# Optimization experiments

Hardware: AMD Instinct MI355X
Metric: run time of the kernel (lower is better)

## Reference

```python
import math
import jax, jax.numpy as jnp
import numpy as np

B, H, W, DIM, HEADS, K = 4, 56, 56, 512, 16, 7


def setup_inputs() -> dict:
    key = jax.random.key(0)
    ks = jax.random.split(key, 8)
    s = 1.0 / math.sqrt(DIM)
    return {
        "hidden_states": jax.random.normal(ks[0], (B, H, W, DIM), jnp.float32),
        "Wq": jax.random.normal(ks[1], (DIM, DIM), jnp.float32) * s,
        "bq": jnp.zeros((DIM,), jnp.float32),
        "Wk": jax.random.normal(ks[2], (DIM, DIM), jnp.float32) * s,
        "bk": jnp.zeros((DIM,), jnp.float32),
        "Wv": jax.random.normal(ks[3], (DIM, DIM), jnp.float32) * s,
        "bv": jnp.zeros((DIM,), jnp.float32),
        "rpb": jax.random.normal(ks[4], (HEADS, 2 * K - 1, 2 * K - 1), jnp.float32) * 0.02,
    }


def reference(hidden_states, Wq, bq, Wk, bk, Wv, bv, rpb):
    b, h_sz, w_sz, dim = hidden_states.shape
    heads = rpb.shape[0]
    k = (rpb.shape[1] + 1) // 2  # rpb is [heads, 2k-1, 2k-1]
    d = dim // heads

    def split_heads(x):
        # [B,H,W,dim] -> [B,heads,H,W,d]  (matches transpose_for_scores permute(0,3,1,2,4))
        return x.reshape(b, h_sz, w_sz, heads, d).transpose(0, 3, 1, 2, 4)

    q = split_heads(hidden_states @ Wq.T + bq) / jnp.sqrt(jnp.asarray(d, hidden_states.dtype))
    key = split_heads(hidden_states @ Wk.T + bk)
    val = split_heads(hidden_states @ Wv.T + bv)

    half = k // 2
    ii = jnp.arange(h_sz)
    ni = jnp.clip(ii - half, 0, h_sz - k)  # neighborhood row start per query row (NATTEN edge clamping)
    jj = jnp.arange(w_sz)
    nj = jnp.clip(jj - half, 0, w_sz - k)

    # natten2dqkrpb: windowed QK with relative position bias (loop over k*k kernel offsets,
    # which mirrors the fused kernel's inner loop and avoids a [B,h,H,W,k,k,d] gather blowup)
    scores = []
    for ki in range(k):
        ridx = ni + ki                      # [H] key row index per query row
        bi = ridx - ii + (k - 1)            # [H] relative bias row index
        key_r = key[:, :, ridx]             # [B,h,H,W,d]
        rpb_r = rpb[:, bi]                  # [h,H,2k-1]
        for kj in range(k):
            cidx = nj + kj                  # [W]
            bj = cidx - jj + (k - 1)        # [W]
            key_rc = key_r[:, :, :, cidx]   # [B,h,H,W,d]
            s = jnp.einsum('bhijd,bhijd->bhij', q, key_rc)
            scores.append(s + rpb_r[:, :, bj][None])  # add bias [1,h,H,W]
    scores = jnp.stack(scores, axis=-1)     # [B,h,H,W,k*k]

    probs = jax.nn.softmax(scores, axis=-1)  # dropout p=0.0 -> identity

    # natten2dav: windowed AV
    ctx = jnp.zeros_like(q)                 # [B,h,H,W,d]
    idx = 0
    for ki in range(k):
        v_r = val[:, :, ni + ki]
        for kj in range(k):
            ctx = ctx + probs[..., idx, None] * v_r[:, :, :, nj + kj]
            idx += 1

    # permute(0,2,3,1,4) then merge heads
    return ctx.transpose(0, 2, 3, 1, 4).reshape(b, h_sz, w_sz, dim)
```

## Files before the change

### kernel.cpp

```cpp
#include <hip/hip_runtime.h>
#include <stdint.h>

typedef unsigned short u16;
typedef __bf16 bf16x8 __attribute__((ext_vector_type(8)));
typedef float f32x4 __attribute__((ext_vector_type(4)));

#define M_PIX 12544
#define DIMC  512
#define NQKV  1536

static __device__ __forceinline__ u16 f2bf(float f) {
  union { float f; uint32_t u; } x; x.f = f;
  uint32_t r = x.u + 0x7FFFu + ((x.u >> 16) & 1u);
  return (u16)(r >> 16);
}

__global__ void cast_all(const float* __restrict__ x, const float* __restrict__ Wq,
                         const float* __restrict__ Wk, const float* __restrict__ Wv,
                         u16* __restrict__ Xb, u16* __restrict__ Wc) {
  int idx = (blockIdx.x * 256 + threadIdx.x) * 4;
  const int NX = M_PIX * DIMC;
  const float* src;
  u16* dst;
  if (idx < NX) {
    src = x + idx; dst = Xb + idx;
  } else {
    int wi = idx - NX;
    if (wi >= NQKV * DIMC) return;
    int r = wi >> 9;
    int c = wi & 511;
    src = (r < 512)  ? (Wq + (size_t)r * 512 + c)
        : (r < 1024) ? (Wk + (size_t)(r - 512) * 512 + c)
                     : (Wv + (size_t)(r - 1024) * 512 + c);
    dst = Wc + wi;
  }
  float4 f = *(const float4*)src;
  uint32_t p0 = (uint32_t)f2bf(f.x) | ((uint32_t)f2bf(f.y) << 16);
  uint32_t p1 = (uint32_t)f2bf(f.z) | ((uint32_t)f2bf(f.w) << 16);
  *(uint2*)dst = make_uint2(p0, p1);
}

__global__ __launch_bounds__(256, 4) void gemm_qkv(
    const u16* __restrict__ A, const u16* __restrict__ Bm,
    const float* __restrict__ bq, const float* __restrict__ bk,
    const float* __restrict__ bv, u16* __restrict__ qkv) {
  __shared__ u16 sA[2][128 * 32];
  __shared__ u16 sB[2][128 * 32];
  const int t = threadIdx.x;
  const int lane = t & 63;
  const int w = t >> 6;
  const int bid = blockIdx.x;
  const int g = (bid & 7) * 147 + (bid >> 3);
  const int tile_m = (g / 12) * 128;
  const int tile_n = (g % 12) * 128;
  const int wm = (w & 1) * 64;
  const int wn = (w >> 1) * 64;
  const int quad = lane >> 4;
  const int l16 = lane & 15;

  f32x4 acc[4][4];
#pragma unroll
  for (int a = 0; a < 4; ++a)
#pragma unroll
    for (int bb = 0; bb < 4; ++bb) acc[a][bb] = (f32x4){0.f, 0.f, 0.f, 0.f};

  const int c0 = t, c1 = t + 256;
  const int r0 = c0 >> 2, ko0 = (((c0 & 3) ^ ((c0 >> 3) & 3))) * 8;
  const int r1 = c1 >> 2, ko1 = (((c1 & 3) ^ ((c1 >> 3) & 3))) * 8;
  const u16* gA0 = A + (size_t)(tile_m + r0) * DIMC + ko0;
  const u16* gA1 = A + (size_t)(tile_m + r1) * DIMC + ko1;
  const u16* gB0 = Bm + (size_t)(tile_n + r0) * DIMC + ko0;
  const u16* gB1 = Bm + (size_t)(tile_n + r1) * DIMC + ko1;
  const int ldsoff = (t & ~63) * 8;

  for (int k0 = 0; k0 < DIMC; k0 += 64) {
#pragma unroll
    for (int h = 0; h < 2; ++h) {
      __builtin_amdgcn_global_load_lds(
          (const __attribute__((address_space(1))) void*)(gA0 + k0 + h * 32),
          (__attribute__((address_space(3))) void*)(sA[h] + 0 * 2048 + ldsoff), 16, 0, 0);
      __builtin_amdgcn_global_load_lds(
          (const __attribute__((address_space(1))) void*)(gA1 + k0 + h * 32),
          (__attribute__((address_space(3))) void*)(sA[h] + 1 * 2048 + ldsoff), 16, 0, 0);
      __builtin_amdgcn_global_load_lds(
          (const __attribute__((address_space(1))) void*)(gB0 + k0 + h * 32),
          (__attribute__((address_space(3))) void*)(sB[h] + 0 * 2048 + ldsoff), 16, 0, 0);
      __builtin_amdgcn_global_load_lds(
          (const __attribute__((address_space(1))) void*)(gB1 + k0 + h * 32),
          (__attribute__((address_space(3))) void*)(sB[h] + 1 * 2048 + ldsoff), 16, 0, 0);
    }
    __syncthreads();

    const int sw8 = (quad ^ ((l16 >> 1) & 3)) * 8;
#pragma unroll
    for (int h = 0; h < 2; ++h) {
      bf16x8 af[4], bfr[4];
#pragma unroll
      for (int mt = 0; mt < 4; ++mt)
        af[mt] = *(const bf16x8*)(sA[h] + (wm + mt * 16 + l16) * 32 + sw8);
#pragma unroll
      for (int nt = 0; nt < 4; ++nt)
        bfr[nt] = *(const bf16x8*)(sB[h] + (wn + nt * 16 + l16) * 32 + sw8);
#pragma unroll
      for (int mt = 0; mt < 4; ++mt)
#pragma unroll
        for (int nt = 0; nt < 4; ++nt)
          acc[mt][nt] = __builtin_amdgcn_mfma_f32_16x16x32_bf16(bfr[nt], af[mt], acc[mt][nt], 0, 0, 0);
    }
    __syncthreads();
  }

  const float qscale = 0.17677669529663687f;
#pragma unroll
  for (int mt = 0; mt < 4; ++mt) {
    const int m = tile_m + wm + mt * 16 + l16;
#pragma unroll
    for (int nt = 0; nt < 4; ++nt) {
      const int n0 = tile_n + wn + nt * 16 + quad * 4;
      const int mat = n0 >> 9;
      const int cc = n0 & 511;
      const float* bias = (mat == 0) ? bq : (mat == 1) ? bk : bv;
      const float4 bv4 = *(const float4*)(bias + cc);
      const float scl = (mat == 0) ? qscale : 1.0f;
      u16 h0 = f2bf((acc[mt][nt][0] + bv4.x) * scl);
      u16 h1 = f2bf((acc[mt][nt][1] + bv4.y) * scl);
      u16 h2 = f2bf((acc[mt][nt][2] + bv4.z) * scl);
      u16 h3 = f2bf((acc[mt][nt][3] + bv4.w) * scl);
      uint2 pk = make_uint2((uint32_t)h0 | ((uint32_t)h1 << 16),
                            (uint32_t)h2 | ((uint32_t)h3 << 16));
      *(uint2*)(qkv + (size_t)mat * M_PIX * DIMC + (size_t)m * DIMC + cc) = pk;
    }
  }
}

__global__ __launch_bounds__(512, 4) void natten_k(const u16* __restrict__ qkv,
                                                   const float* __restrict__ rpb,
                                                   float* __restrict__ out) {
  __shared__ u16 sP[8 * 2688];
  __shared__ u16 sVt[32 * 296];
  __shared__ float sRpb[256];
  __shared__ uint32_t sTbl[320];

  const int tid = threadIdx.x;
  const int lane = tid & 63;
  const int w = tid >> 6;
  const int l16 = lane & 15;
  const int quad = lane >> 4;

  const int bid = blockIdx.x;
  const int xcd = bid & 7;
  const int idx = bid >> 3;
  const int head = idx / 14;
  const int gl = idx - head * 14;
  const int g = xcd * 14 + gl;
  const int jg = g & 3;
  const int gi = g >> 2;
  const int b = gi / 7;
  const int ig = gi - b * 7;
  const int i0 = ig * 8, j0 = jg * 14;
  int c0 = j0 - 3; c0 = c0 < 0 ? 0 : (c0 > 36 ? 36 : c0);
  int nib = i0 - 3; nib = nib < 0 ? 0 : (nib > 49 ? 49 : nib);

  const int iw = i0 + w;
  int niw = iw - 3; niw = niw < 0 ? 0 : (niw > 49 ? 49 : niw);
  const int rowoff = niw - nib;
  const int par = rowoff & 1;
  const int woff2 = rowoff * 20 - par * 4;
  const int wconst = niw - iw + 6;

  const int qv = l16 < 14 ? l16 : 13;
  const int jq = j0 + qv;
  int njq = jq - 3; njq = njq < 0 ? 0 : (njq > 49 ? 49 : njq);
  const uint32_t offq = (uint32_t)(njq - c0);
  const int Cq = wconst * 13 + (c0 - jq + 6);

  const u16* Kpl = qkv + (size_t)M_PIX * DIMC;

  union { uint4 u; bf16x8 v; } qu;
  qu.u = make_uint4(0, 0, 0, 0);
  if (l16 < 14) {
    size_t qpx = (size_t)((b * 56 + iw) * 56 + j0 + l16);
    qu.u = *(const uint4*)(qkv + qpx * DIMC + head * 32 + quad * 8);
  }
  const bf16x8 qf = qu.v;

  if (tid < 296) {
    const int pair = tid >> 1, half = tid & 1;
    const int cand0 = pair * 2;
    int r = (cand0 * 205) >> 12;
    int c = cand0 - r * 20;
    int rimg = nib + r;
    const bool ok = (rimg < 56);
    size_t px = (size_t)((b * 56 + rimg) * 56 + c0 + c);
    const u16* vsrc = Kpl + (size_t)M_PIX * DIMC + px * DIMC + head * 32 + half * 16;
    u16* vt = sVt + cand0;
#pragma unroll
    for (int dgh = 0; dgh < 2; ++dgh) {
      uint4 va = ok ? *(const uint4*)(vsrc + dgh * 8) : make_uint4(0, 0, 0, 0);
      uint4 vb = ok ? *(const uint4*)(vsrc + DIMC + dgh * 8) : make_uint4(0, 0, 0, 0);
      int d0 = (half * 2 + dgh) * 8;
      *(uint32_t*)(vt + (d0 + 0) * 296) = __builtin_amdgcn_perm(vb.x, va.x, 0x05040100u);
      *(uint32_t*)(vt + (d0 + 1) * 296) = __builtin_amdgcn_perm(vb.x, va.x, 0x07060302u);
      *(uint32_t*)(vt + (d0 + 2) * 296) = __builtin_amdgcn_perm(vb.y, va.y, 0x05040100u);
      *(uint32_t*)(vt + (d0 + 3) * 296) = __builtin_amdgcn_perm(vb.y, va.y, 0x07060302u);
      *(uint32_t*)(vt + (d0 + 4) * 296) = __builtin_amdgcn_perm(vb.z, va.z, 0x05040100u);
      *(uint32_t*)(vt + (d0 + 5) * 296) = __builtin_amdgcn_perm(vb.z, va.z, 0x07060302u);
      *(uint32_t*)(vt + (d0 + 6) * 296) = __builtin_amdgcn_perm(vb.w, va.w, 0x05040100u);
      *(uint32_t*)(vt + (d0 + 7) * 296) = __builtin_amdgcn_perm(vb.w, va.w, 0x07060302u);
    }
  }
  const float LOG2E = 1.4426950408889634f;
  if (tid < 256) sRpb[tid] = (tid < 169) ? rpb[head * 169 + tid] * LOG2E : 0.f;
  if (tid < 320) {
    int pp = tid >= 160 ? 1 : 0;
    int s = tid - pp * 160;
    int t0 = s - pp * 4;
    uint32_t e = 255u;
    if (t0 >= 0 && t0 < 140) {
      int r = (t0 * 205) >> 12;
      int c = t0 - r * 20;
      e = (uint32_t)c | ((uint32_t)(r * 13 + c) << 8);
    }
    sTbl[tid] = e;
  }

  const int pxbase = (b * 56 + nib) * 56 + c0;
  const u16* kbase = Kpl + (size_t)head * 32 + quad * 8;
  bf16x8 kreg[9];
#pragma unroll
  for (int ch = 0; ch < 9; ++ch) {
    int cand = woff2 + ch * 16 + l16;
    int r = (cand * 205) >> 12;
    int c = cand - r * 20;
    int px = pxbase + r * 56 + c;
    kreg[ch] = *(const bf16x8*)(kbase + (size_t)px * DIMC);
  }

  __syncthreads();

  u16* sPw = sP + w * 2688;
  f32x4 S[9];
  __builtin_amdgcn_s_setprio(1);
#pragma unroll
  for (int ch = 0; ch < 9; ++ch)
    S[ch] = __builtin_amdgcn_mfma_f32_16x16x32_bf16(kreg[ch], qf, (f32x4){0.f, 0.f, 0.f, 0.f}, 0, 0, 0);
  __builtin_amdgcn_s_setprio(0);

  float l = 0.f;
  const uint32_t* tb = sTbl + par * 160;
#pragma unroll
  for (int ch = 0; ch < 9; ++ch) {
    uint4 te = *(const uint4*)(tb + ch * 16 + quad * 4);
    float pv[4];
    uint32_t es[4] = {te.x, te.y, te.z, te.w};
#pragma unroll
    for (int rg = 0; rg < 4; ++rg) {
      uint32_t e = es[rg];
      uint32_t ce = e & 255u;
      bool valid = (ce - offq) < 7u;
      int ridx = (int)((e >> 8) & 255u) + Cq;
      float rbl = sRpb[ridx];
      float p = exp2f(__builtin_fmaf(S[ch][rg], LOG2E, rbl));
      p = valid ? p : 0.f;
      pv[rg] = p;
      l += p;
    }
    uint32_t plo, phi;
    asm("v_cvt_pk_bf16_f32 %0, %1, %2" : "=v"(plo) : "v"(pv[0]), "v"(pv[1]));
    asm("v_cvt_pk_bf16_f32 %0, %1, %2" : "=v"(phi) : "v"(pv[2]), "v"(pv[3]));
    *(uint2*)((char*)sPw + l16 * 336 + ch * 32 + quad * 8) = make_uint2(plo, phi);
  }
  *(uint2*)((char*)sPw + l16 * 336 + 9 * 32 + quad * 8) = make_uint2(0u, 0u);
  l += __shfl_xor(l, 16);
  l += __shfl_xor(l, 32);

  asm volatile("s_waitcnt lgkmcnt(0)" ::: "memory");
  __builtin_amdgcn_sched_barrier(0);

  f32x4 O0 = (f32x4){0.f, 0.f, 0.f, 0.f};
  f32x4 O1 = (f32x4){0.f, 0.f, 0.f, 0.f};
  __builtin_amdgcn_s_setprio(1);
#pragma unroll
  for (int c32 = 0; c32 < 5; ++c32) {
    bf16x8 pf = *(const bf16x8*)((char*)sPw + l16 * 336 + c32 * 64 + quad * 16);
    bf16x8 v0 = *(const bf16x8*)((char*)sVt + (0 + l16) * 592 + woff2 * 2 + c32 * 64 + quad * 16);
    bf16x8 v1 = *(const bf16x8*)((char*)sVt + (16 + l16) * 592 + woff2 * 2 + c32 * 64 + quad * 16);
    O0 = __builtin_amdgcn_mfma_f32_16x16x32_bf16(v0, pf, O0, 0, 0, 0);
    O1 = __builtin_amdgcn_mfma_f32_16x16x32_bf16(v1, pf, O1, 0, 0, 0);
  }
  __builtin_amdgcn_s_setprio(0);

  if (l16 < 14) {
    const float inv = __builtin_amdgcn_rcpf(l);
    float* op = out + ((size_t)((b * 56 + iw) * 56 + j0 + l16)) * DIMC + head * 32;
    *(float4*)(op + quad * 4) =
        make_float4(O0[0] * inv, O0[1] * inv, O0[2] * inv, O0[3] * inv);
    *(float4*)(op + 16 + quad * 4) =
        make_float4(O1[0] * inv, O1[1] * inv, O1[2] * inv, O1[3] * inv);
  }
}

extern "C" void kernel_launch(void* const* d_in, const int* in_sizes, int n_in,
                              void* d_out, int out_size, void* d_ws, size_t ws_size,
                              hipStream_t stream) {
  const float* x   = (const float*)d_in[0];
  const float* Wq  = (const float*)d_in[1];
  const float* bq  = (const float*)d_in[2];
  const float* Wk  = (const float*)d_in[3];
  const float* bk  = (const float*)d_in[4];
  const float* Wv  = (const float*)d_in[5];
  const float* bv  = (const float*)d_in[6];
  const float* rpb = (const float*)d_in[7];
  float* out = (float*)d_out;

  u16* Xb  = (u16*)d_ws;
  u16* Wc  = Xb + (size_t)M_PIX * DIMC;
  u16* qkv = Wc + (size_t)NQKV * DIMC;

  const int ncast = (M_PIX * DIMC + NQKV * DIMC) / 4;
  cast_all<<<(ncast + 255) / 256, 256, 0, stream>>>(x, Wq, Wk, Wv, Xb, Wc);
  gemm_qkv<<<1176, 256, 0, stream>>>(Xb, Wc, bq, bk, bv, qkv);
  natten_k<<<1792, 512, 0, stream>>>(qkv, rpb, out);
}
```

Measured before the change: 147.9 us.

## Fuse fp32-to-bf16 activation cast into QKV GEMM A-tile loads

Removes the separate cast pass over the activations. The GEMM now reads fp32 X directly, converts it with v_cvt_pk_bf16_f32 in registers, and writes swizzled bf16 into LDS; only the weights still go through a standalone cast kernel. This avoids writing and re-reading a 12.8 MB bf16 intermediate. In exchange, the A operand is no longer loaded asynchronously with global_load_lds, so the GEMM reads twice the bytes per A element (each fp32 tile is re-read by the 12 N-tiles) and spends more registers and VALU work in the load path.

```diff
diff --git a/kernel.cpp b/kernel.cpp
--- a/kernel.cpp
+++ b/kernel.cpp
@@ -15,33 +15,23 @@
   return (u16)(r >> 16);
 }
 
-__global__ void cast_all(const float* __restrict__ x, const float* __restrict__ Wq,
-                         const float* __restrict__ Wk, const float* __restrict__ Wv,
-                         u16* __restrict__ Xb, u16* __restrict__ Wc) {
-  int idx = (blockIdx.x * 256 + threadIdx.x) * 4;
-  const int NX = M_PIX * DIMC;
-  const float* src;
-  u16* dst;
-  if (idx < NX) {
-    src = x + idx; dst = Xb + idx;
-  } else {
-    int wi = idx - NX;
-    if (wi >= NQKV * DIMC) return;
-    int r = wi >> 9;
-    int c = wi & 511;
-    src = (r < 512)  ? (Wq + (size_t)r * 512 + c)
-        : (r < 1024) ? (Wk + (size_t)(r - 512) * 512 + c)
-                     : (Wv + (size_t)(r - 1024) * 512 + c);
-    dst = Wc + wi;
-  }
+__global__ void cast_w(const float* __restrict__ Wq, const float* __restrict__ Wk,
+                       const float* __restrict__ Wv, u16* __restrict__ Wc) {
+  int wi = (blockIdx.x * 256 + threadIdx.x) * 4;
+  if (wi >= NQKV * DIMC) return;
+  int r = wi >> 9;
+  int c = wi & 511;
+  const float* src = (r < 512)  ? (Wq + (size_t)r * 512 + c)
+                   : (r < 1024) ? (Wk + (size_t)(r - 512) * 512 + c)
+                                : (Wv + (size_t)(r - 1024) * 512 + c);
   float4 f = *(const float4*)src;
   uint32_t p0 = (uint32_t)f2bf(f.x) | ((uint32_t)f2bf(f.y) << 16);
   uint32_t p1 = (uint32_t)f2bf(f.z) | ((uint32_t)f2bf(f.w) << 16);
-  *(uint2*)dst = make_uint2(p0, p1);
+  *(uint2*)(Wc + wi) = make_uint2(p0, p1);
 }
 
 __global__ __launch_bounds__(256, 4) void gemm_qkv(
-    const u16* __restrict__ A, const u16* __restrict__ Bm,
+    const float* __restrict__ X, const u16* __restrict__ Bm,
     const float* __restrict__ bq, const float* __restrict__ bk,
     const float* __restrict__ bv, u16* __restrict__ qkv) {
   __shared__ u16 sA[2][128 * 32];
@@ -65,23 +55,38 @@
     for (int bb = 0; bb < 4; ++bb) acc[a][bb] = (f32x4){0.f, 0.f, 0.f, 0.f};
 
   const int c0 = t, c1 = t + 256;
-  const int r0 = c0 >> 2, ko0 = (((c0 & 3) ^ ((c0 >> 3) & 3))) * 8;
-  const int r1 = c1 >> 2, ko1 = (((c1 & 3) ^ ((c1 >> 3) & 3))) * 8;
-  const u16* gA0 = A + (size_t)(tile_m + r0) * DIMC + ko0;
-  const u16* gA1 = A + (size_t)(tile_m + r1) * DIMC + ko1;
+  const int r0 = c0 >> 2, j0c = c0 & 3;
+  const int r1 = c1 >> 2, j1c = c1 & 3;
+  const int s0 = j0c ^ ((c0 >> 3) & 3);
+  const int s1 = j1c ^ ((c1 >> 3) & 3);
+  const float* gX0 = X + (size_t)(tile_m + r0) * DIMC + j0c * 8;
+  const float* gX1 = X + (size_t)(tile_m + r1) * DIMC + j1c * 8;
+  const int ko0 = s0 * 8, ko1 = s1 * 8;
   const u16* gB0 = Bm + (size_t)(tile_n + r0) * DIMC + ko0;
   const u16* gB1 = Bm + (size_t)(tile_n + r1) * DIMC + ko1;
   const int ldsoff = (t & ~63) * 8;
+  u16* const dA0 = (u16*)sA[0] + r0 * 32 + s0 * 8;
+  u16* const dA1 = (u16*)sA[0] + r1 * 32 + s1 * 8;
+  const int halfStride = 128 * 32;
 
   for (int k0 = 0; k0 < DIMC; k0 += 64) {
 #pragma unroll
     for (int h = 0; h < 2; ++h) {
-      __builtin_amdgcn_global_load_lds(
-          (const __attribute__((address_space(1))) void*)(gA0 + k0 + h * 32),
-          (__attribute__((address_space(3))) void*)(sA[h] + 0 * 2048 + ldsoff), 16, 0, 0);
-      __builtin_amdgcn_global_load_lds(
-          (const __attribute__((address_space(1))) void*)(gA1 + k0 + h * 32),
-          (__attribute__((address_space(3))) void*)(sA[h] + 1 * 2048 + ldsoff), 16, 0, 0);
+      float4 xa0 = *(const float4*)(gX0 + k0 + h * 32);
+      float4 xb0 = *(const float4*)(gX0 + k0 + h * 32 + 4);
+      float4 xa1 = *(const float4*)(gX1 + k0 + h * 32);
+      float4 xb1 = *(const float4*)(gX1 + k0 + h * 32 + 4);
+      uint32_t w0, w1, w2, w3, y0, y1, y2, y3;
+      asm("v_cvt_pk_bf16_f32 %0, %1, %2" : "=v"(w0) : "v"(xa0.x), "v"(xa0.y));
+      asm("v_cvt_pk_bf16_f32 %0, %1, %2" : "=v"(w1) : "v"(xa0.z), "v"(xa0.w));
+      asm("v_cvt_pk_bf16_f32 %0, %1, %2" : "=v"(w2) : "v"(xb0.x), "v"(xb0.y));
+      asm("v_cvt_pk_bf16_f32 %0, %1, %2" : "=v"(w3) : "v"(xb0.z), "v"(xb0.w));
+      asm("v_cvt_pk_bf16_f32 %0, %1, %2" : "=v"(y0) : "v"(xa1.x), "v"(xa1.y));
+      asm("v_cvt_pk_bf16_f32 %0, %1, %2" : "=v"(y1) : "v"(xa1.z), "v"(xa1.w));
+      asm("v_cvt_pk_bf16_f32 %0, %1, %2" : "=v"(y2) : "v"(xb1.x), "v"(xb1.y));
+      asm("v_cvt_pk_bf16_f32 %0, %1, %2" : "=v"(y3) : "v"(xb1.z), "v"(xb1.w));
+      *(uint4*)(dA0 + h * halfStride) = make_uint4(w0, w1, w2, w3);
+      *(uint4*)(dA1 + h * halfStride) = make_uint4(y0, y1, y2, y3);
       __builtin_amdgcn_global_load_lds(
           (const __attribute__((address_space(1))) void*)(gB0 + k0 + h * 32),
           (__attribute__((address_space(3))) void*)(sB[h] + 0 * 2048 + ldsoff), 16, 0, 0);
@@ -313,12 +318,11 @@
   const float* rpb = (const float*)d_in[7];
   float* out = (float*)d_out;
 
-  u16* Xb  = (u16*)d_ws;
-  u16* Wc  = Xb + (size_t)M_PIX * DIMC;
+  u16* Wc  = (u16*)d_ws;
   u16* qkv = Wc + (size_t)NQKV * DIMC;
 
-  const int ncast = (M_PIX * DIMC + NQKV * DIMC) / 4;
-  cast_all<<<(ncast + 255) / 256, 256, 0, stream>>>(x, Wq, Wk, Wv, Xb, Wc);
-  gemm_qkv<<<1176, 256, 0, stream>>>(Xb, Wc, bq, bk, bv, qkv);
+  const int ncast = (NQKV * DIMC) / 4;
+  cast_w<<<(ncast + 255) / 256, 256, 0, stream>>>(Wq, Wk, Wv, Wc);
+  gemm_qkv<<<1176, 256, 0, stream>>>(x, Wc, bq, bk, bv, qkv);
   natten_k<<<1792, 512, 0, stream>>>(qkv, rpb, out);
 }
```

Measured after the change: 169.3 us. +14.5%, slower.
